# Optimization experiments

Hardware: AMD Instinct MI355X
Metric: run time of the kernel (lower is better)

Reference implementation:

```python
import jax, jax.numpy as jnp
import numpy as np

NUM_HEADS = 12
HEAD_SIZE = 64
HIDDEN = 768


def setup_inputs() -> dict:
    key = jax.random.key(0)
    ks = jax.random.split(key, 5)
    B, S, H = 2, 2048, HIDDEN
    scale_in = 0.02
    return {
        "x": jax.random.normal(ks[0], (B, S, H), dtype=jnp.float32),
        "w_qkv": jax.random.normal(ks[1], (3 * H, H), dtype=jnp.float32) * scale_in,
        "b_qkv": jax.random.normal(ks[2], (3 * H,), dtype=jnp.float32) * scale_in,
        "w_o": jax.random.normal(ks[3], (H, H), dtype=jnp.float32) * scale_in,
        "b_o": jax.random.normal(ks[4], (H,), dtype=jnp.float32) * scale_in,
    }


def reference(x, w_qkv, b_qkv, w_o, b_o):
    B, S, H = x.shape
    nh, hd = NUM_HEADS, HEAD_SIZE
    qkv = x @ w_qkv.T + b_qkv                      # (B, S, 3H)
    Q, K, V = jnp.split(qkv, 3, axis=-1)
    Q = Q.reshape(B, S, nh, hd)
    K = K.reshape(B, S, nh, hd)
    V = V.reshape(B, S, nh, hd)
    # scores: (B, nh, S_q, S_k)
    scores = jnp.einsum('bqhd,bkhd->bhqk', Q, K)
    causal = jnp.triu(jnp.ones((S, S), dtype=bool), k=1)
    scores = jnp.where(causal, -jnp.inf, scores)
    attn = jax.nn.softmax(scores / jnp.sqrt(jnp.float32(hd)), axis=3)
    out = jnp.einsum('bhqk,bkhd->bqhd', attn, V).reshape(B, S, nh * hd)
    return out @ w_o.T + b_o
```

## Files before the change

### kernel.cpp

```cpp
#include <hip/hip_runtime.h>
#include <stdint.h>


#define B_   2
#define S_   2048
#define H_   768
#define NH_  12
#define HD_  64
#define M_   4096
#define K_   768
#define N_QKV 2304
#define QKV_ELEMS (B_*NH_*S_*HD_)
#define SCL_ 0.18033688f

using bf16x8 = __attribute__((ext_vector_type(8))) __bf16;
using f32x4  = __attribute__((ext_vector_type(4))) float;
using f32x16 = __attribute__((ext_vector_type(16))) float;

__device__ inline unsigned short f2bf(float f) {
  unsigned int u = __float_as_uint(f);
  u = (u + 0x7FFFu + ((u >> 16) & 1u)) >> 16;
  return (unsigned short)u;
}
__device__ inline float fexp2(float x) {
  float r; asm("v_exp_f32 %0, %1" : "=v"(r) : "v"(x)); return r;
}
__device__ inline unsigned cvtpk(float lo, float hi) {
  unsigned r; asm("v_cvt_pk_bf16_f32 %0, %1, %2" : "=v"(r) : "v"(lo), "v"(hi)); return r;
}
__device__ inline void gload_lds16(const void* g, void* l) {
  __builtin_amdgcn_global_load_lds((const __attribute__((address_space(1))) void*)g,
                                   (__attribute__((address_space(3))) void*)l, 16, 0, 0);
}
#define VWAIT0() do { asm volatile("s_waitcnt vmcnt(0)" ::: "memory"); \
                      __builtin_amdgcn_sched_barrier(0); } while (0)
#define LWAIT0() do { asm volatile("s_waitcnt lgkmcnt(0)" ::: "memory"); \
                      __builtin_amdgcn_sched_barrier(0); } while (0)

__global__ void cast3(const float* __restrict__ s0, unsigned short* __restrict__ d0, int n0f,
                      const float* __restrict__ s1, unsigned short* __restrict__ d1, int n1f,
                      const float* __restrict__ s2, unsigned short* __restrict__ d2, int n2f) {
  int i = blockIdx.x * blockDim.x + threadIdx.x;
  const float* s; unsigned short* d; int j;
  if (i < n0f)                { s = s0; d = d0; j = i; }
  else if (i < n0f + n1f)     { s = s1; d = d1; j = i - n0f; }
  else if (i < n0f + n1f + n2f) { s = s2; d = d2; j = i - n0f - n1f; }
  else return;
  float4 v = reinterpret_cast<const float4*>(s)[j];
  ushort4 o;
  o.x = f2bf(v.x); o.y = f2bf(v.y); o.z = f2bf(v.z); o.w = f2bf(v.w);
  reinterpret_cast<ushort4*>(d)[j] = o;
}

template<int N, int MODE, int GX>
__global__ __launch_bounds__(256, 3)
void gemm_nt(const unsigned short* __restrict__ A,
             const unsigned short* __restrict__ Bw,
             const float* __restrict__ bias,
             unsigned short* __restrict__ qkv_base,
             float* __restrict__ outp)
{
  __shared__ unsigned short As[128*32];
  __shared__ unsigned short Bs[128*32];
  const int tid  = threadIdx.x;
  const int lane = tid & 63;
  const int wid  = tid >> 6;
  const int g = lane >> 4, lr = lane & 15;
  const int wm = wid >> 1, wn = wid & 1;
  const int cpx = (GX * 32) >> 3;
  const int id  = blockIdx.x;
  const int sw  = (id & 7) * cpx + (id >> 3);
  const int n0 = (sw % GX) * 128;
  const int m0 = (sw / GX) * 128;

  f32x4 acc[4][4];
  #pragma unroll
  for (int i = 0; i < 4; ++i)
    #pragma unroll
    for (int j = 0; j < 4; ++j) acc[i][j] = f32x4{0.f, 0.f, 0.f, 0.f};

  for (int k0 = 0; k0 < K_; k0 += 32) {
    #pragma unroll
    for (int it = 0; it < 2; ++it) {
      int c = it*256 + wid*64 + lane;
      int row = c >> 2, seg = c & 3;
      int lb = __builtin_amdgcn_readfirstlane((it*256 + wid*64) * 8);
      gload_lds16(&A [(size_t)(m0 + row) * K_ + k0 + seg*8], &As[lb]);
      gload_lds16(&Bw[(size_t)(n0 + row) * K_ + k0 + seg*8], &Bs[lb]);
    }
    __syncthreads();
    bf16x8 af[4], bfr[4];
    #pragma unroll
    for (int i = 0; i < 4; ++i) {
      int ra = wm*64 + i*16 + lr;
      af[i]  = *reinterpret_cast<const bf16x8*>(&As[ra*32 + g*8]);
      int rb = wn*64 + i*16 + lr;
      bfr[i] = *reinterpret_cast<const bf16x8*>(&Bs[rb*32 + g*8]);
    }
    #pragma unroll
    for (int i = 0; i < 4; ++i)
      #pragma unroll
      for (int j = 0; j < 4; ++j)
        acc[i][j] = __builtin_amdgcn_mfma_f32_16x16x32_bf16(af[i], bfr[j], acc[i][j], 0, 0, 0);
    __syncthreads();
  }

  #pragma unroll
  for (int j = 0; j < 4; ++j) {
    int col = n0 + wn*64 + j*16 + lr;
    float bv = bias[col];
    if constexpr (MODE == 0) {
      int which = col / 768;
      int rem = col - which * 768;
      int h = rem >> 6, d = rem & 63;
      if (which == 0) {
        unsigned short* dst = qkv_base;
        #pragma unroll
        for (int i = 0; i < 4; ++i)
          #pragma unroll
          for (int r = 0; r < 4; ++r) {
            int rowm = m0 + wm*64 + i*16 + g*4 + r;
            int bb = rowm >> 11, ss = rowm & 2047;
            dst[(((size_t)(bb*NH_ + h))*S_ + ss)*HD_ + d] = f2bf(acc[i][j][r] + bv);
          }
      } else if (which == 1) {
        unsigned short* dst = qkv_base + (size_t)QKV_ELEMS;
        #pragma unroll
        for (int i = 0; i < 4; ++i)
          #pragma unroll
          for (int r = 0; r < 4; ++r) {
            int rowm = m0 + wm*64 + i*16 + g*4 + r;
            int bb = rowm >> 11, ss = rowm & 2047;
            size_t byteoff = ((size_t)(bb*NH_ + h)*(S_>>5) + (ss>>5))*4096
                           + (size_t)(((d>>3)*32 + (ss&31))*16 + (d&7)*2);
            dst[byteoff >> 1] = f2bf(acc[i][j][r] + bv);
          }
      } else {
        unsigned short* dst = qkv_base + 2*(size_t)QKV_ELEMS;
        #pragma unroll
        for (int i = 0; i < 4; ++i) {
          int rowm = m0 + wm*64 + i*16 + g*4;
          int bb = rowm >> 11, ss = rowm & 2047;
          unsigned w0 = (unsigned)f2bf(acc[i][j][0] + bv) | ((unsigned)f2bf(acc[i][j][1] + bv) << 16);
          unsigned w1 = (unsigned)f2bf(acc[i][j][2] + bv) | ((unsigned)f2bf(acc[i][j][3] + bv) << 16);
          uint2 u; u.x = w0; u.y = w1;
          size_t byteoff = ((size_t)(bb*NH_ + h)*(S_>>5) + (ss>>5))*4096
                         + (size_t)((((ss&31)>>3)*64 + d)*16 + (ss&7)*2);
          *reinterpret_cast<uint2*>(&dst[byteoff >> 1]) = u;
        }
      }
    } else {
      #pragma unroll
      for (int i = 0; i < 4; ++i)
        #pragma unroll
        for (int r = 0; r < 4; ++r) {
          int rowm = m0 + wm*64 + i*16 + g*4 + r;
          outp[(size_t)rowm * H_ + col] = acc[i][j][r] + bv;
        }
    }
  }
}

__global__ __launch_bounds__(256, 3)
void attn_fwd(const unsigned short* __restrict__ Qp,
              const unsigned short* __restrict__ Ktp,
              const unsigned short* __restrict__ Vtp,
              unsigned short* __restrict__ attn)
{
  __shared__ __align__(16) char smem[33792];
  float* mlb = (float*)(smem + 32768);

  const int tid = threadIdx.x;
  const int l = tid & 63, w = tid >> 6;
  const int q31 = l & 31, hi = l >> 5;
  const int idx = blockIdx.x;
  const int bh = (idx & 7) + 8 * ((idx >> 3) % 3);
  const int pr = (idx >> 3) / 3;
  const unsigned short* Qh = Qp + (size_t)bh * S_ * HD_;
  const char* Ktb = (const char*)Ktp + (size_t)bh * (S_>>5) * 4096;
  const char* Vtb = (const char*)Vtp + (size_t)bh * (S_>>5) * 4096;
  const int bb = bh / NH_, hh = bh % NH_;

  unsigned short* Kl = (unsigned short*)(smem + w*8192);
  unsigned short* Vl = Kl + 2048;
  float* OscW = (float*)(smem + w*8192);

  for (int qi = 0; qi < 2; ++qi) {
    const int qt = qi ? pr : (63 - pr);
    const int qrow = qt*32 + q31;

    bf16x8 qf[4];
    #pragma unroll
    for (int ks = 0; ks < 4; ++ks)
      qf[ks] = *reinterpret_cast<const bf16x8*>(&Qh[(size_t)qrow*HD_ + ks*16 + hi*8]);

    f32x16 oacc0, oacc1;
    #pragma unroll
    for (int r = 0; r < 16; ++r) { oacc0[r] = 0.f; oacc1[r] = 0.f; }
    float lrun = 0.f;

    const int p = w;
    const int nt = (qt >= p) ? ((qt - p) >> 2) + 1 : 0;
    const bool dw = ((qt & 3) == p);
    const int ntm1 = nt - 1;

    const char* kt = Ktb + (size_t)p*4096 + l*16;
    const char* vt = Vtb + (size_t)p*4096 + l*16;

    auto STAGE = [&]() {
      gload_lds16(kt,        Kl);
      gload_lds16(kt + 1024, Kl + 512);
      gload_lds16(kt + 2048, Kl + 1024);
      gload_lds16(kt + 3072, Kl + 1536);
      gload_lds16(vt,        Vl);
      gload_lds16(vt + 1024, Vl + 512);
      gload_lds16(vt + 2048, Vl + 1024);
      gload_lds16(vt + 3072, Vl + 1536);
      kt += 16384; vt += 16384;
    };

    if (nt > 0) STAGE();

    for (int i = 0; i < nt; ++i) {
      VWAIT0();
      bf16x8 k0 = *reinterpret_cast<const bf16x8*>(&Kl[((0+hi)*32 + q31)*8]);
      bf16x8 k1 = *reinterpret_cast<const bf16x8*>(&Kl[((2+hi)*32 + q31)*8]);
      bf16x8 k2 = *reinterpret_cast<const bf16x8*>(&Kl[((4+hi)*32 + q31)*8]);
      bf16x8 k3 = *reinterpret_cast<const bf16x8*>(&Kl[((6+hi)*32 + q31)*8]);
      bf16x8 v0 = *reinterpret_cast<const bf16x8*>(&Vl[((  hi)*64 +      q31)*8]);
      bf16x8 v1 = *reinterpret_cast<const bf16x8*>(&Vl[((2+hi)*64 +      q31)*8]);
      bf16x8 v2 = *reinterpret_cast<const bf16x8*>(&Vl[((  hi)*64 + 32 + q31)*8]);
      bf16x8 v3 = *reinterpret_cast<const bf16x8*>(&Vl[((2+hi)*64 + 32 + q31)*8]);
      LWAIT0();
      if (i + 1 < nt) STAGE();
      asm volatile("" ::: "memory");

      f32x16 sf;
      #pragma unroll
      for (int r = 0; r < 16; ++r) sf[r] = 0.f;
      sf = __builtin_amdgcn_mfma_f32_32x32x16_bf16(k0, qf[0], sf, 0, 0, 0);
      sf = __builtin_amdgcn_mfma_f32_32x32x16_bf16(k1, qf[1], sf, 0, 0, 0);
      sf = __builtin_amdgcn_mfma_f32_32x32x16_bf16(k2, qf[2], sf, 0, 0, 0);
      sf = __builtin_amdgcn_mfma_f32_32x32x16_bf16(k3, qf[3], sf, 0, 0, 0);

      if (dw && i == ntm1) {
        const int kv0 = qt*32;
        #pragma unroll
        for (int r = 0; r < 16; ++r) {
          int kv = kv0 + (r & 3) + 8*(r >> 2) + 4*hi;
          if (kv > qrow) sf[r] = -1e38f;
        }
      }

      #pragma unroll
      for (int r = 0; r < 16; ++r)
        sf[r] = fexp2(sf[r] * SCL_);
      float s0 = (sf[0]  + sf[1])  + (sf[2]  + sf[3]);
      float s1 = (sf[4]  + sf[5])  + (sf[6]  + sf[7]);
      float s2 = (sf[8]  + sf[9])  + (sf[10] + sf[11]);
      float s3 = (sf[12] + sf[13]) + (sf[14] + sf[15]);
      lrun += (s0 + s1) + (s2 + s3);

      unsigned pw0 = cvtpk(sf[0],  sf[1]);
      unsigned pw1 = cvtpk(sf[2],  sf[3]);
      unsigned pw2 = cvtpk(sf[4],  sf[5]);
      unsigned pw3 = cvtpk(sf[6],  sf[7]);
      unsigned pw4 = cvtpk(sf[8],  sf[9]);
      unsigned pw5 = cvtpk(sf[10], sf[11]);
      unsigned pw6 = cvtpk(sf[12], sf[13]);
      unsigned pw7 = cvtpk(sf[14], sf[15]);
      asm("v_permlane32_swap_b32 %0, %1" : "+v"(pw0), "+v"(pw2));
      asm("v_permlane32_swap_b32 %0, %1" : "+v"(pw1), "+v"(pw3));
      asm("v_permlane32_swap_b32 %0, %1" : "+v"(pw4), "+v"(pw6));
      asm("v_permlane32_swap_b32 %0, %1" : "+v"(pw5), "+v"(pw7));
      uint4 pf0; pf0.x = pw0; pf0.y = pw1; pf0.z = pw2; pf0.w = pw3;
      uint4 pf1; pf1.x = pw4; pf1.y = pw5; pf1.z = pw6; pf1.w = pw7;

      oacc0 = __builtin_amdgcn_mfma_f32_32x32x16_bf16(
          v0, *reinterpret_cast<bf16x8*>(&pf0), oacc0, 0, 0, 0);
      oacc0 = __builtin_amdgcn_mfma_f32_32x32x16_bf16(
          v1, *reinterpret_cast<bf16x8*>(&pf1), oacc0, 0, 0, 0);
      oacc1 = __builtin_amdgcn_mfma_f32_32x32x16_bf16(
          v2, *reinterpret_cast<bf16x8*>(&pf0), oacc1, 0, 0, 0);
      oacc1 = __builtin_amdgcn_mfma_f32_32x32x16_bf16(
          v3, *reinterpret_cast<bf16x8*>(&pf1), oacc1, 0, 0, 0);
    }

    const int q = tid & 31, dseg8 = tid >> 5;
    __syncthreads();

    #pragma unroll
    for (int rr = 0; rr < 4; ++rr) {
      f32x4 a;
      #pragma unroll
      for (int e = 0; e < 4; ++e) a[e] = oacc0[4*rr + e];
      *reinterpret_cast<f32x4*>(&OscW[q31*36 + 8*rr + 4*hi]) = a;
    }
    mlb[w*64 + hi*32 + q31] = lrun;
    __syncthreads();

    float inv;
    {
      float lt = (mlb[q] + mlb[32+q]) + (mlb[64+q] + mlb[96+q])
               + (mlb[128+q] + mlb[160+q]) + (mlb[192+q] + mlb[224+q]);
      inv = 1.f / lt;
    }
    if (dseg8 < 4) {
      const int dd = dseg8*8;
      #define OSC(a, off) (*reinterpret_cast<f32x4*>((float*)(smem + (a)*8192) + (off)))
      f32x4 a0 = OSC(0, q*36 + dd), b0 = OSC(0, q*36 + dd + 4);
      f32x4 a1 = OSC(1, q*36 + dd), b1 = OSC(1, q*36 + dd + 4);
      f32x4 a2 = OSC(2, q*36 + dd), b2 = OSC(2, q*36 + dd + 4);
      f32x4 a3 = OSC(3, q*36 + dd), b3 = OSC(3, q*36 + dd + 4);
      f32x4 ra, rb;
      #pragma unroll
      for (int e = 0; e < 4; ++e) {
        ra[e] = ((a0[e] + a1[e]) + (a2[e] + a3[e])) * inv;
        rb[e] = ((b0[e] + b1[e]) + (b2[e] + b3[e])) * inv;
      }
      uint4 ov;
      ov.x = cvtpk(ra[0], ra[1]); ov.y = cvtpk(ra[2], ra[3]);
      ov.z = cvtpk(rb[0], rb[1]); ov.w = cvtpk(rb[2], rb[3]);
      *reinterpret_cast<uint4*>(&attn[((size_t)(bb*S_ + qt*32 + q))*H_ + hh*HD_ + dd]) = ov;
    }
    __syncthreads();

    #pragma unroll
    for (int rr = 0; rr < 4; ++rr) {
      f32x4 a;
      #pragma unroll
      for (int e = 0; e < 4; ++e) a[e] = oacc1[4*rr + e];
      *reinterpret_cast<f32x4*>(&OscW[q31*36 + 8*rr + 4*hi]) = a;
    }
    __syncthreads();

    if (dseg8 >= 4) {
      const int dd = (dseg8 - 4)*8;
      f32x4 a0 = OSC(0, q*36 + dd), b0 = OSC(0, q*36 + dd + 4);
      f32x4 a1 = OSC(1, q*36 + dd), b1 = OSC(1, q*36 + dd + 4);
      f32x4 a2 = OSC(2, q*36 + dd), b2 = OSC(2, q*36 + dd + 4);
      f32x4 a3 = OSC(3, q*36 + dd), b3 = OSC(3, q*36 + dd + 4);
      #undef OSC
      f32x4 ra, rb;
      #pragma unroll
      for (int e = 0; e < 4; ++e) {
        ra[e] = ((a0[e] + a1[e]) + (a2[e] + a3[e])) * inv;
        rb[e] = ((b0[e] + b1[e]) + (b2[e] + b3[e])) * inv;
      }
      uint4 ov;
      ov.x = cvtpk(ra[0], ra[1]); ov.y = cvtpk(ra[2], ra[3]);
      ov.z = cvtpk(rb[0], rb[1]); ov.w = cvtpk(rb[2], rb[3]);
      *reinterpret_cast<uint4*>(&attn[((size_t)(bb*S_ + qt*32 + q))*H_ + hh*HD_ + 32 + dd]) = ov;
    }
    __syncthreads();
  }
}

extern "C" void kernel_launch(void* const* d_in, const int* in_sizes, int n_in,
                              void* d_out, int out_size, void* d_ws, size_t ws_size,
                              hipStream_t stream)
{
  const float* x      = (const float*)d_in[0];
  const float* w_qkv  = (const float*)d_in[1];
  const float* b_qkv  = (const float*)d_in[2];
  const float* w_o    = (const float*)d_in[3];
  const float* b_o    = (const float*)d_in[4];
  float* out = (float*)d_out;

  unsigned short* xb    = (unsigned short*)d_ws;
  unsigned short* wqkvb = xb    + (size_t)M_ * K_;
  unsigned short* wob   = wqkvb + (size_t)N_QKV * K_;
  unsigned short* Qw    = wob   + (size_t)H_ * H_;
  unsigned short* Ktw   = Qw + (size_t)QKV_ELEMS;
  unsigned short* Vtw   = Ktw + (size_t)QKV_ELEMS;
  unsigned short* attn  = Vtw + (size_t)QKV_ELEMS;

  cast3<<<5376, 256, 0, stream>>>(x, xb, 786432,
                                  w_qkv, wqkvb, 442368,
                                  w_o, wob, 147456);
  gemm_nt<N_QKV, 0, 18><<<576, 256, 0, stream>>>(xb, wqkvb, b_qkv, Qw, nullptr);
  attn_fwd<<<dim3(768), 256, 0, stream>>>(Qw, Ktw, Vtw, attn);
  gemm_nt<H_, 1, 6><<<192, 256, 0, stream>>>(attn, wob, b_o, nullptr, out);
}
```

Measured before the change: 79.14 us.

## Process paired high and low query tiles together sharing K/V loads

The attention kernel used to process its two query tiles (a late one and an early one) one after the other, staging K/V twice. Now both tiles are handled in a single pass over the K/V tiles, and the low tile's MFMAs are predicated to stop once its causal range ends. This halves K/V global-to-LDS traffic for the shared prefix and keeps more independent MFMA work in flight per iteration. In exchange it doubles the accumulator registers, so launch bounds drop from 3 to 2 blocks per CU, which may cut occupancy.

```diff
diff --git a/kernel.cpp b/kernel.cpp
--- a/kernel.cpp
+++ b/kernel.cpp
@@ -161,13 +161,13 @@
   }
 }
 
-__global__ __launch_bounds__(256, 3)
+__global__ __launch_bounds__(256, 2)
 void attn_fwd(const unsigned short* __restrict__ Qp,
               const unsigned short* __restrict__ Ktp,
               const unsigned short* __restrict__ Vtp,
               unsigned short* __restrict__ attn)
 {
-  __shared__ __align__(16) char smem[33792];
+  __shared__ __align__(16) char smem[34816];
   float* mlb = (float*)(smem + 32768);
 
   const int tid = threadIdx.x;
@@ -185,120 +185,157 @@
   unsigned short* Vl = Kl + 2048;
   float* OscW = (float*)(smem + w*8192);
 
-  for (int qi = 0; qi < 2; ++qi) {
-    const int qt = qi ? pr : (63 - pr);
-    const int qrow = qt*32 + q31;
-
-    bf16x8 qf[4];
-    #pragma unroll
-    for (int ks = 0; ks < 4; ++ks)
-      qf[ks] = *reinterpret_cast<const bf16x8*>(&Qh[(size_t)qrow*HD_ + ks*16 + hi*8]);
-
-    f32x16 oacc0, oacc1;
-    #pragma unroll
-    for (int r = 0; r < 16; ++r) { oacc0[r] = 0.f; oacc1[r] = 0.f; }
-    float lrun = 0.f;
-
-    const int p = w;
-    const int nt = (qt >= p) ? ((qt - p) >> 2) + 1 : 0;
-    const bool dw = ((qt & 3) == p);
-    const int ntm1 = nt - 1;
-
-    const char* kt = Ktb + (size_t)p*4096 + l*16;
-    const char* vt = Vtb + (size_t)p*4096 + l*16;
-
-    auto STAGE = [&]() {
-      gload_lds16(kt,        Kl);
-      gload_lds16(kt + 1024, Kl + 512);
-      gload_lds16(kt + 2048, Kl + 1024);
-      gload_lds16(kt + 3072, Kl + 1536);
-      gload_lds16(vt,        Vl);
-      gload_lds16(vt + 1024, Vl + 512);
-      gload_lds16(vt + 2048, Vl + 1024);
-      gload_lds16(vt + 3072, Vl + 1536);
-      kt += 16384; vt += 16384;
-    };
-
-    if (nt > 0) STAGE();
-
-    for (int i = 0; i < nt; ++i) {
-      VWAIT0();
-      bf16x8 k0 = *reinterpret_cast<const bf16x8*>(&Kl[((0+hi)*32 + q31)*8]);
-      bf16x8 k1 = *reinterpret_cast<const bf16x8*>(&Kl[((2+hi)*32 + q31)*8]);
-      bf16x8 k2 = *reinterpret_cast<const bf16x8*>(&Kl[((4+hi)*32 + q31)*8]);
-      bf16x8 k3 = *reinterpret_cast<const bf16x8*>(&Kl[((6+hi)*32 + q31)*8]);
-      bf16x8 v0 = *reinterpret_cast<const bf16x8*>(&Vl[((  hi)*64 +      q31)*8]);
-      bf16x8 v1 = *reinterpret_cast<const bf16x8*>(&Vl[((2+hi)*64 +      q31)*8]);
-      bf16x8 v2 = *reinterpret_cast<const bf16x8*>(&Vl[((  hi)*64 + 32 + q31)*8]);
-      bf16x8 v3 = *reinterpret_cast<const bf16x8*>(&Vl[((2+hi)*64 + 32 + q31)*8]);
-      LWAIT0();
-      if (i + 1 < nt) STAGE();
-      asm volatile("" ::: "memory");
-
-      f32x16 sf;
-      #pragma unroll
-      for (int r = 0; r < 16; ++r) sf[r] = 0.f;
-      sf = __builtin_amdgcn_mfma_f32_32x32x16_bf16(k0, qf[0], sf, 0, 0, 0);
-      sf = __builtin_amdgcn_mfma_f32_32x32x16_bf16(k1, qf[1], sf, 0, 0, 0);
-      sf = __builtin_amdgcn_mfma_f32_32x32x16_bf16(k2, qf[2], sf, 0, 0, 0);
-      sf = __builtin_amdgcn_mfma_f32_32x32x16_bf16(k3, qf[3], sf, 0, 0, 0);
-
-      if (dw && i == ntm1) {
-        const int kv0 = qt*32;
-        #pragma unroll
-        for (int r = 0; r < 16; ++r) {
-          int kv = kv0 + (r & 3) + 8*(r >> 2) + 4*hi;
-          if (kv > qrow) sf[r] = -1e38f;
-        }
+  const int qtH = 63 - pr, qtL = pr;
+  const int qrowH = qtH*32 + q31, qrowL = qtL*32 + q31;
+
+  bf16x8 qfH[4], qfL[4];
+  #pragma unroll
+  for (int ks = 0; ks < 4; ++ks) {
+    qfH[ks] = *reinterpret_cast<const bf16x8*>(&Qh[(size_t)qrowH*HD_ + ks*16 + hi*8]);
+    qfL[ks] = *reinterpret_cast<const bf16x8*>(&Qh[(size_t)qrowL*HD_ + ks*16 + hi*8]);
+  }
+
+  f32x16 oH0, oH1, oL0, oL1;
+  #pragma unroll
+  for (int r = 0; r < 16; ++r) { oH0[r]=0.f; oH1[r]=0.f; oL0[r]=0.f; oL1[r]=0.f; }
+  float lrunH = 0.f, lrunL = 0.f;
+
+  const int p = w;
+  const int ntH = ((qtH - p) >> 2) + 1;
+  const int ntL = (qtL >= p) ? ((qtL - p) >> 2) + 1 : 0;
+  const bool dwH = ((qtH & 3) == p);
+  const bool dwL = ((qtL & 3) == p);
+  const int ntHm1 = ntH - 1, ntLm1 = ntL - 1;
+
+  const char* kt = Ktb + (size_t)p*4096 + l*16;
+  const char* vt = Vtb + (size_t)p*4096 + l*16;
+
+  auto STAGE = [&]() {
+    gload_lds16(kt,        Kl);
+    gload_lds16(kt + 1024, Kl + 512);
+    gload_lds16(kt + 2048, Kl + 1024);
+    gload_lds16(kt + 3072, Kl + 1536);
+    gload_lds16(vt,        Vl);
+    gload_lds16(vt + 1024, Vl + 512);
+    gload_lds16(vt + 2048, Vl + 1024);
+    gload_lds16(vt + 3072, Vl + 1536);
+    kt += 16384; vt += 16384;
+  };
+
+  STAGE();
+
+  for (int i = 0; i < ntH; ++i) {
+    VWAIT0();
+    bf16x8 k0 = *reinterpret_cast<const bf16x8*>(&Kl[((0+hi)*32 + q31)*8]);
+    bf16x8 k1 = *reinterpret_cast<const bf16x8*>(&Kl[((2+hi)*32 + q31)*8]);
+    bf16x8 k2 = *reinterpret_cast<const bf16x8*>(&Kl[((4+hi)*32 + q31)*8]);
+    bf16x8 k3 = *reinterpret_cast<const bf16x8*>(&Kl[((6+hi)*32 + q31)*8]);
+    bf16x8 v0 = *reinterpret_cast<const bf16x8*>(&Vl[((  hi)*64 +      q31)*8]);
+    bf16x8 v1 = *reinterpret_cast<const bf16x8*>(&Vl[((2+hi)*64 +      q31)*8]);
+    bf16x8 v2 = *reinterpret_cast<const bf16x8*>(&Vl[((  hi)*64 + 32 + q31)*8]);
+    bf16x8 v3 = *reinterpret_cast<const bf16x8*>(&Vl[((2+hi)*64 + 32 + q31)*8]);
+    LWAIT0();
+    if (i + 1 < ntH) STAGE();
+    asm volatile("" ::: "memory");
+
+    const bool doL = (i < ntL);
+
+    f32x16 sfH;
+    #pragma unroll
+    for (int r = 0; r < 16; ++r) sfH[r] = 0.f;
+    sfH = __builtin_amdgcn_mfma_f32_32x32x16_bf16(k0, qfH[0], sfH, 0, 0, 0);
+    sfH = __builtin_amdgcn_mfma_f32_32x32x16_bf16(k1, qfH[1], sfH, 0, 0, 0);
+    sfH = __builtin_amdgcn_mfma_f32_32x32x16_bf16(k2, qfH[2], sfH, 0, 0, 0);
+    sfH = __builtin_amdgcn_mfma_f32_32x32x16_bf16(k3, qfH[3], sfH, 0, 0, 0);
+    f32x16 sfL;
+    #pragma unroll
+    for (int r = 0; r < 16; ++r) sfL[r] = 0.f;
+    if (doL) {
+      sfL = __builtin_amdgcn_mfma_f32_32x32x16_bf16(k0, qfL[0], sfL, 0, 0, 0);
+      sfL = __builtin_amdgcn_mfma_f32_32x32x16_bf16(k1, qfL[1], sfL, 0, 0, 0);
+      sfL = __builtin_amdgcn_mfma_f32_32x32x16_bf16(k2, qfL[2], sfL, 0, 0, 0);
+      sfL = __builtin_amdgcn_mfma_f32_32x32x16_bf16(k3, qfL[3], sfL, 0, 0, 0);
+    }
+
+    if (dwH && i == ntHm1) {
+      const int kv0 = qtH*32;
+      #pragma unroll
+      for (int r = 0; r < 16; ++r) {
+        int kv = kv0 + (r & 3) + 8*(r >> 2) + 4*hi;
+        if (kv > qrowH) sfH[r] = -1e38f;
       }
-
-      #pragma unroll
-      for (int r = 0; r < 16; ++r)
-        sf[r] = fexp2(sf[r] * SCL_);
-      float s0 = (sf[0]  + sf[1])  + (sf[2]  + sf[3]);
-      float s1 = (sf[4]  + sf[5])  + (sf[6]  + sf[7]);
-      float s2 = (sf[8]  + sf[9])  + (sf[10] + sf[11]);
-      float s3 = (sf[12] + sf[13]) + (sf[14] + sf[15]);
-      lrun += (s0 + s1) + (s2 + s3);
-
-      unsigned pw0 = cvtpk(sf[0],  sf[1]);
-      unsigned pw1 = cvtpk(sf[2],  sf[3]);
-      unsigned pw2 = cvtpk(sf[4],  sf[5]);
-      unsigned pw3 = cvtpk(sf[6],  sf[7]);
-      unsigned pw4 = cvtpk(sf[8],  sf[9]);
-      unsigned pw5 = cvtpk(sf[10], sf[11]);
-      unsigned pw6 = cvtpk(sf[12], sf[13]);
-      unsigned pw7 = cvtpk(sf[14], sf[15]);
+    }
+    if (doL && dwL && i == ntLm1) {
+      const int kv0 = qtL*32;
+      #pragma unroll
+      for (int r = 0; r < 16; ++r) {
+        int kv = kv0 + (r & 3) + 8*(r >> 2) + 4*hi;
+        if (kv > qrowL) sfL[r] = -1e38f;
+      }
+    }
+
+    #pragma unroll
+    for (int r = 0; r < 16; ++r) sfH[r] = fexp2(sfH[r] * SCL_);
+    {
+      float s0 = (sfH[0]+sfH[1])+(sfH[2]+sfH[3]);
+      float s1 = (sfH[4]+sfH[5])+(sfH[6]+sfH[7]);
+      float s2 = (sfH[8]+sfH[9])+(sfH[10]+sfH[11]);
+      float s3 = (sfH[12]+sfH[13])+(sfH[14]+sfH[15]);
+      lrunH += (s0+s1)+(s2+s3);
+      unsigned pw0 = cvtpk(sfH[0],sfH[1]),  pw1 = cvtpk(sfH[2],sfH[3]);
+      unsigned pw2 = cvtpk(sfH[4],sfH[5]),  pw3 = cvtpk(sfH[6],sfH[7]);
+      unsigned pw4 = cvtpk(sfH[8],sfH[9]),  pw5 = cvtpk(sfH[10],sfH[11]);
+      unsigned pw6 = cvtpk(sfH[12],sfH[13]), pw7 = cvtpk(sfH[14],sfH[15]);
       asm("v_permlane32_swap_b32 %0, %1" : "+v"(pw0), "+v"(pw2));
       asm("v_permlane32_swap_b32 %0, %1" : "+v"(pw1), "+v"(pw3));
       asm("v_permlane32_swap_b32 %0, %1" : "+v"(pw4), "+v"(pw6));
       asm("v_permlane32_swap_b32 %0, %1" : "+v"(pw5), "+v"(pw7));
       uint4 pf0; pf0.x = pw0; pf0.y = pw1; pf0.z = pw2; pf0.w = pw3;
       uint4 pf1; pf1.x = pw4; pf1.y = pw5; pf1.z = pw6; pf1.w = pw7;
-
-      oacc0 = __builtin_amdgcn_mfma_f32_32x32x16_bf16(
-          v0, *reinterpret_cast<bf16x8*>(&pf0), oacc0, 0, 0, 0);
-      oacc0 = __builtin_amdgcn_mfma_f32_32x32x16_bf16(
-          v1, *reinterpret_cast<bf16x8*>(&pf1), oacc0, 0, 0, 0);
-      oacc1 = __builtin_amdgcn_mfma_f32_32x32x16_bf16(
-          v2, *reinterpret_cast<bf16x8*>(&pf0), oacc1, 0, 0, 0);
-      oacc1 = __builtin_amdgcn_mfma_f32_32x32x16_bf16(
-          v3, *reinterpret_cast<bf16x8*>(&pf1), oacc1, 0, 0, 0);
-    }
-
-    const int q = tid & 31, dseg8 = tid >> 5;
-    __syncthreads();
-
+      oH0 = __builtin_amdgcn_mfma_f32_32x32x16_bf16(v0, *reinterpret_cast<bf16x8*>(&pf0), oH0, 0, 0, 0);
+      oH0 = __builtin_amdgcn_mfma_f32_32x32x16_bf16(v1, *reinterpret_cast<bf16x8*>(&pf1), oH0, 0, 0, 0);
+      oH1 = __builtin_amdgcn_mfma_f32_32x32x16_bf16(v2, *reinterpret_cast<bf16x8*>(&pf0), oH1, 0, 0, 0);
+      oH1 = __builtin_amdgcn_mfma_f32_32x32x16_bf16(v3, *reinterpret_cast<bf16x8*>(&pf1), oH1, 0, 0, 0);
+    }
+
+    if (doL) {
+      #pragma unroll
+      for (int r = 0; r < 16; ++r) sfL[r] = fexp2(sfL[r] * SCL_);
+      float s0 = (sfL[0]+sfL[1])+(sfL[2]+sfL[3]);
+      float s1 = (sfL[4]+sfL[5])+(sfL[6]+sfL[7]);
+      float s2 = (sfL[8]+sfL[9])+(sfL[10]+sfL[11]);
+      float s3 = (sfL[12]+sfL[13])+(sfL[14]+sfL[15]);
+      lrunL += (s0+s1)+(s2+s3);
+      unsigned pw0 = cvtpk(sfL[0],sfL[1]),  pw1 = cvtpk(sfL[2],sfL[3]);
+      unsigned pw2 = cvtpk(sfL[4],sfL[5]),  pw3 = cvtpk(sfL[6],sfL[7]);
+      unsigned pw4 = cvtpk(sfL[8],sfL[9]),  pw5 = cvtpk(sfL[10],sfL[11]);
+      unsigned pw6 = cvtpk(sfL[12],sfL[13]), pw7 = cvtpk(sfL[14],sfL[15]);
+      asm("v_permlane32_swap_b32 %0, %1" : "+v"(pw0), "+v"(pw2));
+      asm("v_permlane32_swap_b32 %0, %1" : "+v"(pw1), "+v"(pw3));
+      asm("v_permlane32_swap_b32 %0, %1" : "+v"(pw4), "+v"(pw6));
+      asm("v_permlane32_swap_b32 %0, %1" : "+v"(pw5), "+v"(pw7));
+      uint4 pf0; pf0.x = pw0; pf0.y = pw1; pf0.z = pw2; pf0.w = pw3;
+      uint4 pf1; pf1.x = pw4; pf1.y = pw5; pf1.z = pw6; pf1.w = pw7;
+      oL0 = __builtin_amdgcn_mfma_f32_32x32x16_bf16(v0, *reinterpret_cast<bf16x8*>(&pf0), oL0, 0, 0, 0);
+      oL0 = __builtin_amdgcn_mfma_f32_32x32x16_bf16(v1, *reinterpret_cast<bf16x8*>(&pf1), oL0, 0, 0, 0);
+      oL1 = __builtin_amdgcn_mfma_f32_32x32x16_bf16(v2, *reinterpret_cast<bf16x8*>(&pf0), oL1, 0, 0, 0);
+      oL1 = __builtin_amdgcn_mfma_f32_32x32x16_bf16(v3, *reinterpret_cast<bf16x8*>(&pf1), oL1, 0, 0, 0);
+    }
+  }
+
+  const int q = tid & 31, dseg8 = tid >> 5;
+
+  auto MERGE = [&](const f32x16& a0v, const f32x16& a1v, float lr, int qt) {
+    __syncthreads();
     #pragma unroll
     for (int rr = 0; rr < 4; ++rr) {
       f32x4 a;
       #pragma unroll
-      for (int e = 0; e < 4; ++e) a[e] = oacc0[4*rr + e];
+      for (int e = 0; e < 4; ++e) a[e] = a0v[4*rr + e];
       *reinterpret_cast<f32x4*>(&OscW[q31*36 + 8*rr + 4*hi]) = a;
     }
-    mlb[w*64 + hi*32 + q31] = lrun;
-    __syncthreads();
-
+    mlb[w*64 + hi*32 + q31] = lr;
+    __syncthreads();
     float inv;
     {
       float lt = (mlb[q] + mlb[32+q]) + (mlb[64+q] + mlb[96+q])
@@ -324,16 +361,14 @@
       *reinterpret_cast<uint4*>(&attn[((size_t)(bb*S_ + qt*32 + q))*H_ + hh*HD_ + dd]) = ov;
     }
     __syncthreads();
-
     #pragma unroll
     for (int rr = 0; rr < 4; ++rr) {
       f32x4 a;
       #pragma unroll
-      for (int e = 0; e < 4; ++e) a[e] = oacc1[4*rr + e];
+      for (int e = 0; e < 4; ++e) a[e] = a1v[4*rr + e];
       *reinterpret_cast<f32x4*>(&OscW[q31*36 + 8*rr + 4*hi]) = a;
     }
     __syncthreads();
-
     if (dseg8 >= 4) {
       const int dd = (dseg8 - 4)*8;
       f32x4 a0 = OSC(0, q*36 + dd), b0 = OSC(0, q*36 + dd + 4);
@@ -353,7 +388,10 @@
       *reinterpret_cast<uint4*>(&attn[((size_t)(bb*S_ + qt*32 + q))*H_ + hh*HD_ + 32 + dd]) = ov;
     }
     __syncthreads();
-  }
+  };
+
+  MERGE(oH0, oH1, lrunH, qtH);
+  MERGE(oL0, oL1, lrunL, qtL);
 }
 
 extern "C" void kernel_launch(void* const* d_in, const int* in_sizes, int n_in,
```

New measurement: 78.85 us. About the same (-0.4%).
